# Performance work log

Hardware: AMD Instinct MI355X
Metric: run time of the kernel (lower is better)

The kernel has to match this reference:

```python
import math
import jax, jax.numpy as jnp
import numpy as np

G, PQ, PV = 12, 4, 8

def setup_inputs() -> dict:
    key = jax.random.key(0)
    ks = jax.random.split(key, 14)
    N, L, Cn, Ce, Ch = 1, 512, 384, 128, 192
    Node = jax.random.normal(ks[0], (N, L, Cn), jnp.float32)
    Edge = jax.random.normal(ks[1], (N, L, L, Ce), jnp.float32)
    # proper rotation matrices via QR of random gaussians
    raw = jax.random.normal(ks[2], (N, L, 3, 3), jnp.float32)
    rots, _ = jnp.linalg.qr(raw)
    trans = jax.random.normal(ks[3], (N, L, 3), jnp.float32) * 10.0
    def lin(k, fan_in, fan_out):
        return jax.random.normal(k, (fan_in, fan_out), jnp.float32) / np.sqrt(fan_in)
    return {
        'Node': Node, 'Edge': Edge, 'rots': rots, 'trans': trans,
        'Wq': lin(ks[4], Cn, Ch), 'Wk': lin(ks[5], Cn, Ch), 'Wv': lin(ks[6], Cn, Ch),
        'Wqv': lin(ks[7], Cn, 3 * G * PQ), 'Wkv': lin(ks[8], Cn, 3 * G * PQ),
        'Wvv': lin(ks[9], Cn, 3 * G * PV), 'Wbias': lin(ks[10], Ce, G),
        'gamma': jnp.zeros((G,), jnp.float32),
        'Wout': lin(ks[11], Ce * G + Ch + G * PV * 4, Cn),
        'bout': jnp.zeros((Cn,), jnp.float32),
    }

def reference(Node, Edge, rots, trans, Wq, Wk, Wv, Wqv, Wkv, Wvv, Wbias, gamma, Wout, bout):
    N, L, Cn = Node.shape
    Ce = Edge.shape[-1]
    Ch = Wq.shape[1]
    ppg = Ch // G
    t = trans / 10.0  # Frame(T.rots, T.trans / 10.0)
    q = (Node @ Wq).reshape(N, L, G, ppg)
    k = (Node @ Wk).reshape(N, L, G, ppg)
    v = (Node @ Wv).reshape(N, L, G, ppg)
    qv = (Node @ Wqv).reshape(N, L, G, PQ, 3)
    kv = (Node @ Wkv).reshape(N, L, G, PQ, 3)
    vv = (Node @ Wvv).reshape(N, L, G, PV, 3)
    apply_frame = lambda p: jnp.einsum('nlij,nlgpj->nlgpi', rots, p) + t[:, :, None, None]
    qv = apply_frame(qv)
    kv = apply_frame(kv)
    vv = apply_frame(vv)
    # pairwise squared point distances, summed over xyz and query points -> [N,L,L,G]
    d = qv[:, :, None] - kv[:, None]
    sq = jnp.sum(d * d, axis=(-1, -2))
    bias = jnp.einsum('nijc,cg->nijg', Edge, Wbias)
    WC = math.sqrt(2.0 / 9.0 / PQ)
    WL = math.sqrt(1.0 / 3.0)
    attn = jnp.einsum('nlgc,nmgc->nlmg', q, k) / math.sqrt(ppg) + bias
    attn = attn - jax.nn.softplus(gamma) * (WC / 2.0) * sq
    attn = jax.nn.softmax(WL * attn, axis=2)  # softmax over key index m
    O_Edge = jnp.einsum('nijg,nijc->nigc', attn, Edge).reshape(N, L, G * Ce)
    O_Node = jnp.einsum('nijg,njgc->nigc', attn, v).reshape(N, L, Ch)
    O_vec = jnp.einsum('nijg,njgpc->nigpc', attn, vv)
    # invert_apply: R^T (x - t)
    O_vec = jnp.einsum('nlji,nlgpj->nlgpi', rots, O_vec - t[:, :, None, None])
    O_norm = jnp.sqrt(jnp.sum(O_vec * O_vec, axis=-1) + 1e-8).reshape(N, L, -1)
    O_vec = O_vec.reshape(N, L, -1)
    feat = jnp.concatenate([O_Edge, O_Node, O_vec, O_norm], axis=-1)
    return feat @ Wout + bout
```

## Files before the change

kernel.cpp:

```cpp
#include <hip/hip_runtime.h>
#include <math.h>

#define LQ 512
#define CN 384
#define CE 128
#define CH 192
#define NG 12
#define PPG 16
#define FEAT 2112
#define NPROJ 1152

#define WS_RAW  0u
#define WS_QVG  589824u
#define WS_KVT  663552u
#define WS_VVG  737280u
#define WS_QN   884736u
#define WS_KNT  890880u
#define WS_KT   897024u
#define WS_ATT  995328u
#define WS_FEAT 4141056u
#define WS_PART 5222400u
#define WS_PM   WS_PART
#define WS_PS   (WS_PART + 12288u)

__global__ __launch_bounds__(256) void k1a_gemm(
    const float* __restrict__ Node,
    const float* __restrict__ Wq, const float* __restrict__ Wk,
    const float* __restrict__ Wv, const float* __restrict__ Wqv,
    const float* __restrict__ Wkv, const float* __restrict__ Wvv,
    float* __restrict__ ws)
{
    __shared__ float As[64][68];
    __shared__ float Bs[64][48];
    const int tid = threadIdx.x;
    const int cb = blockIdx.x % 24;
    const int l0 = (blockIdx.x / 24) * 64;
    const int col0 = cb * 48;

    const float* W; int nc, lc0;
    if (col0 < 192)      { W = Wq;  nc = 192; lc0 = col0; }
    else if (col0 < 384) { W = Wk;  nc = 192; lc0 = col0 - 192; }
    else if (col0 < 576) { W = Wv;  nc = 192; lc0 = col0 - 384; }
    else if (col0 < 720) { W = Wqv; nc = 144; lc0 = col0 - 576; }
    else if (col0 < 864) { W = Wkv; nc = 144; lc0 = col0 - 720; }
    else                 { W = Wvv; nc = 288; lc0 = col0 - 864; }

    const int tx = tid & 15, ty = tid >> 4;
    float acc[4][3];
#pragma unroll
    for (int r = 0; r < 4; ++r)
#pragma unroll
        for (int c = 0; c < 3; ++c) acc[r][c] = 0.f;

    for (int kc = 0; kc < 6; ++kc) {
        __syncthreads();
#pragma unroll
        for (int pass = 0; pass < 4; ++pass) {
            int m = (tid >> 4) + pass * 16;
            int kk = (tid & 15) * 4;
            const float4 a = *(const float4*)(Node + (size_t)(l0 + m) * CN + kc * 64 + kk);
            As[kk + 0][m] = a.x; As[kk + 1][m] = a.y;
            As[kk + 2][m] = a.z; As[kk + 3][m] = a.w;
        }
#pragma unroll
        for (int p = 0; p < 12; ++p) {
            int idx = p * 256 + tid;
            int kk = idx / 48, c = idx - kk * 48;
            Bs[kk][c] = W[(size_t)(kc * 64 + kk) * nc + lc0 + c];
        }
        __syncthreads();
#pragma unroll 8
        for (int kk = 0; kk < 64; ++kk) {
            const float4 av = *(const float4*)&As[kk][tx * 4];
            const float b0 = Bs[kk][ty * 3 + 0];
            const float b1 = Bs[kk][ty * 3 + 1];
            const float b2 = Bs[kk][ty * 3 + 2];
            acc[0][0] = fmaf(av.x, b0, acc[0][0]); acc[0][1] = fmaf(av.x, b1, acc[0][1]); acc[0][2] = fmaf(av.x, b2, acc[0][2]);
            acc[1][0] = fmaf(av.y, b0, acc[1][0]); acc[1][1] = fmaf(av.y, b1, acc[1][1]); acc[1][2] = fmaf(av.y, b2, acc[1][2]);
            acc[2][0] = fmaf(av.z, b0, acc[2][0]); acc[2][1] = fmaf(av.z, b1, acc[2][1]); acc[2][2] = fmaf(av.z, b2, acc[2][2]);
            acc[3][0] = fmaf(av.w, b0, acc[3][0]); acc[3][1] = fmaf(av.w, b1, acc[3][1]); acc[3][2] = fmaf(av.w, b2, acc[3][2]);
        }
    }
    float* raw = ws + WS_RAW;
#pragma unroll
    for (int r = 0; r < 4; ++r)
#pragma unroll
        for (int c = 0; c < 3; ++c)
            raw[(size_t)(l0 + tx * 4 + r) * NPROJ + col0 + ty * 3 + c] = acc[r][c];
    if (col0 >= 192 && col0 < 384) {
#pragma unroll
        for (int r = 0; r < 4; ++r)
#pragma unroll
            for (int c = 0; c < 3; ++c)
                ws[WS_KT + (size_t)(col0 - 192 + ty * 3 + c) * LQ + l0 + tx * 4 + r] = acc[r][c];
    }
}

__global__ __launch_bounds__(256) void k1b_vec(
    const float* __restrict__ rots, const float* __restrict__ trans,
    float* __restrict__ ws)
{
    __shared__ float sqbuf[96];
    const int tid = threadIdx.x;
    const int l = blockIdx.x;
    const float* raw = ws + WS_RAW + (size_t)l * NPROJ;

    if (tid < 192) {
        int src, pt, typ;
        if (tid < 48)      { typ = 0; pt = tid;      src = 576 + pt * 3; }
        else if (tid < 96) { typ = 1; pt = tid - 48; src = 720 + pt * 3; }
        else               { typ = 2; pt = tid - 96; src = 864 + pt * 3; }
        float v0 = raw[src], v1 = raw[src + 1], v2 = raw[src + 2];
        const float* R = rots + l * 9;
        float o0 = R[0] * v0 + R[1] * v1 + R[2] * v2 + trans[l * 3 + 0] * 0.1f;
        float o1 = R[3] * v0 + R[4] * v1 + R[5] * v2 + trans[l * 3 + 1] * 0.1f;
        float o2 = R[6] * v0 + R[7] * v1 + R[8] * v2 + trans[l * 3 + 2] * 0.1f;
        if (typ == 0) {
            float* dst = ws + WS_QVG + (size_t)l * 144 + pt * 3;
            dst[0] = o0; dst[1] = o1; dst[2] = o2;
        } else if (typ == 1) {
            ws[WS_KVT + (size_t)(pt * 3 + 0) * LQ + l] = o0;
            ws[WS_KVT + (size_t)(pt * 3 + 1) * LQ + l] = o1;
            ws[WS_KVT + (size_t)(pt * 3 + 2) * LQ + l] = o2;
        } else {
            float* dst = ws + WS_VVG + (size_t)l * 288 + pt * 3;
            dst[0] = o0; dst[1] = o1; dst[2] = o2;
        }
        if (tid < 96) sqbuf[tid] = o0 * o0 + o1 * o1 + o2 * o2;
    }
    __syncthreads();
    if (tid < 24) {
        int typ = tid / 12, g = tid % 12;
        int b = typ * 48 + g * 4;
        float s = sqbuf[b] + sqbuf[b + 1] + sqbuf[b + 2] + sqbuf[b + 3];
        if (typ == 0) ws[WS_QN + (size_t)l * 12 + g] = s;
        else          ws[WS_KNT + (size_t)g * LQ + l] = s;
    }
}

__global__ __launch_bounds__(256, 3) void k2_attn(
    const float* __restrict__ Edge, const float* __restrict__ Wbias,
    const float* __restrict__ gamma, float* __restrict__ ws)
{
    __shared__ float et[256 * 33];
    __shared__ float wbs[CE * NG];
    __shared__ float qls[CH], qvls[144], qnls[NG], cgls[NG];
    __shared__ float red[4][NG];
    const int tid = threadIdx.x;
    const int i = blockIdx.x >> 1;
    const int h = blockIdx.x & 1;
    const int j = h * 256 + tid;

    for (int u = tid; u < CE * NG; u += 256) wbs[u] = Wbias[u];
    if (tid < CH)  qls[tid]  = ws[WS_RAW + (size_t)i * NPROJ + tid];
    if (tid < 144) qvls[tid] = ws[WS_QVG + (size_t)i * 144 + tid];
    if (tid < NG) {
        qnls[tid] = ws[WS_QN + (size_t)i * NG + tid];
        cgls[tid] = log1pf(__expf(gamma[tid])) * 0.11785113019775793f;
    }
    __syncthreads();

    float lgs[NG];
    {
        const float* KT  = ws + WS_KT;
        const float* KVT = ws + WS_KVT;
        const float* KNT = ws + WS_KNT;
#pragma unroll
        for (int g = 0; g < NG; ++g) {
            float qk = 0.f;
#pragma unroll
            for (int u = 0; u < PPG; ++u)
                qk = fmaf(qls[g * PPG + u], KT[(size_t)(g * PPG + u) * LQ + j], qk);
            float dt = 0.f;
#pragma unroll
            for (int u = 0; u < 12; ++u)
                dt = fmaf(qvls[g * 12 + u], KVT[(size_t)(g * 12 + u) * LQ + j], dt);
            float sq = qnls[g] + KNT[(size_t)g * LQ + j] - 2.f * dt;
            lgs[g] = qk * 0.25f - cgls[g] * sq;
        }
    }

    const float4* e4 = (const float4*)Edge + ((size_t)i * LQ + h * 256) * 32;
    for (int ch = 0; ch < 4; ++ch) {
        __syncthreads();
#pragma unroll
        for (int kk = 0; kk < 8; ++kk) {
            int idx = kk * 256 + tid;
            int jr = idx >> 3, c4 = idx & 7;
            float4 v = e4[(size_t)jr * 32 + ch * 8 + c4];
            float* d = et + jr * 33 + c4 * 4;
            d[0] = v.x; d[1] = v.y; d[2] = v.z; d[3] = v.w;
        }
        __syncthreads();
        const float* wbch = wbs + ch * 32 * NG;
        const float* r0 = et + tid * 33;
#pragma unroll 4
        for (int c = 0; c < 32; ++c) {
            float e0 = r0[c];
            const float* wb = wbch + c * NG;
#pragma unroll
            for (int g = 0; g < NG; ++g) lgs[g] = fmaf(e0, wb[g], lgs[g]);
        }
    }

    const float WL = 0.5773502691896258f;
    const int wid = tid >> 6, lane = tid & 63;
    float pm[NG];
#pragma unroll
    for (int g = 0; g < NG; ++g) pm[g] = lgs[g];
#pragma unroll
    for (int g = 0; g < NG; ++g)
        for (int off = 1; off < 64; off <<= 1)
            pm[g] = fmaxf(pm[g], __shfl_xor(pm[g], off));
    if (lane == 0) {
#pragma unroll
        for (int g = 0; g < NG; ++g) red[wid][g] = pm[g];
    }
    __syncthreads();
    float gm[NG];
#pragma unroll
    for (int g = 0; g < NG; ++g)
        gm[g] = fmaxf(fmaxf(red[0][g], red[1][g]), fmaxf(red[2][g], red[3][g]));
    if (tid < NG)
        ws[WS_PM + ((size_t)i * 2 + h) * NG + tid] =
            fmaxf(fmaxf(red[0][tid], red[1][tid]), fmaxf(red[2][tid], red[3][tid]));
    __syncthreads();

    float ps[NG];
#pragma unroll
    for (int g = 0; g < NG; ++g) {
        float e = __expf(WL * (lgs[g] - gm[g]));
        lgs[g] = e;
        ps[g] = e;
    }
#pragma unroll
    for (int g = 0; g < NG; ++g)
        for (int off = 1; off < 64; off <<= 1)
            ps[g] += __shfl_xor(ps[g], off);
    if (lane == 0) {
#pragma unroll
        for (int g = 0; g < NG; ++g) red[wid][g] = ps[g];
    }
    __syncthreads();
    if (tid < NG)
        ws[WS_PS + ((size_t)i * 2 + h) * NG + tid] =
            red[0][tid] + red[1][tid] + red[2][tid] + red[3][tid];

    float4* dst = (float4*)(ws + WS_ATT + ((size_t)i * LQ + j) * NG);
    float4 s0, s1, s2;
    s0.x = lgs[0]; s0.y = lgs[1]; s0.z = lgs[2];  s0.w = lgs[3];
    s1.x = lgs[4]; s1.y = lgs[5]; s1.z = lgs[6];  s1.w = lgs[7];
    s2.x = lgs[8]; s2.y = lgs[9]; s2.z = lgs[10]; s2.w = lgs[11];
    dst[0] = s0; dst[1] = s1; dst[2] = s2;
}

__global__ __launch_bounds__(256) void k3_out(
    const float* __restrict__ Edge, const float* __restrict__ rots,
    const float* __restrict__ trans, float* __restrict__ ws)
{
    __shared__ float at[LQ][13];
    __shared__ float bufA[4][32][NG][4];
    __shared__ float ovec[288];
    __shared__ float sc[2][NG];
    const int tid = threadIdx.x;
    const int qi = blockIdx.x;
    const float* att = ws + WS_ATT + (size_t)qi * LQ * NG;

    if (tid < 24) {
        const float WL = 0.5773502691896258f;
        int hh = tid / NG, g = tid % NG;
        float m0 = ws[WS_PM + ((size_t)qi * 2 + 0) * NG + g];
        float m1 = ws[WS_PM + ((size_t)qi * 2 + 1) * NG + g];
        float ss0 = ws[WS_PS + ((size_t)qi * 2 + 0) * NG + g];
        float ss1 = ws[WS_PS + ((size_t)qi * 2 + 1) * NG + g];
        float m = fmaxf(m0, m1);
        float e0 = __expf(WL * (m0 - m));
        float e1 = __expf(WL * (m1 - m));
        float denom = ss0 * e0 + ss1 * e1;
        sc[hh][g] = (hh ? e1 : e0) / denom;
    }
    __syncthreads();

    for (int m = 0; m < 2; ++m) {
        int j = tid + m * 256;
        int hh = j >> 8;
        const float4* src = (const float4*)(att + (size_t)j * NG);
        float4 a = src[0], b = src[1], c = src[2];
        at[j][0] = a.x * sc[hh][0]; at[j][1] = a.y * sc[hh][1];
        at[j][2] = a.z * sc[hh][2]; at[j][3] = a.w * sc[hh][3];
        at[j][4] = b.x * sc[hh][4]; at[j][5] = b.y * sc[hh][5];
        at[j][6] = b.z * sc[hh][6]; at[j][7] = b.w * sc[hh][7];
        at[j][8] = c.x * sc[hh][8]; at[j][9] = c.y * sc[hh][9];
        at[j][10] = c.z * sc[hh][10]; at[j][11] = c.w * sc[hh][11];
    }
    __syncthreads();

    const int w = tid >> 6, lane = tid & 63, jh = lane >> 5, c4 = lane & 31;
    float acc[NG][4];
#pragma unroll
    for (int g = 0; g < NG; ++g)
#pragma unroll
        for (int r = 0; r < 4; ++r) acc[g][r] = 0.f;
    const float4* e4 = (const float4*)(Edge + (size_t)qi * LQ * CE);
    for (int jj = 0; jj < 64; ++jj) {
        int j = w * 128 + jh * 64 + jj;
        float4 e = e4[(size_t)j * 32 + c4];
#pragma unroll
        for (int g = 0; g < NG; ++g) {
            float a = at[j][g];
            acc[g][0] = fmaf(a, e.x, acc[g][0]);
            acc[g][1] = fmaf(a, e.y, acc[g][1]);
            acc[g][2] = fmaf(a, e.z, acc[g][2]);
            acc[g][3] = fmaf(a, e.w, acc[g][3]);
        }
    }
#pragma unroll
    for (int g = 0; g < NG; ++g)
#pragma unroll
        for (int r = 0; r < 4; ++r) acc[g][r] += __shfl_xor(acc[g][r], 32);
    if (jh == 0) {
#pragma unroll
        for (int g = 0; g < NG; ++g)
#pragma unroll
            for (int r = 0; r < 4; ++r) bufA[w][c4][g][r] = acc[g][r];
    }
    __syncthreads();
    float* feat = ws + WS_FEAT + (size_t)qi * FEAT;
    for (int m = 0; m < 6; ++m) {
        int o = tid + m * 256;
        int g = o >> 7, c = o & 127;
        int cc4 = c >> 2, r = c & 3;
        feat[o] = bufA[0][cc4][g][r] + bufA[1][cc4][g][r] +
                  bufA[2][cc4][g][r] + bufA[3][cc4][g][r];
    }

    const float* raw = ws + WS_RAW;
    const float* vvg = ws + WS_VVG;
    for (int ph = 0; ph < 2; ++ph) {
        int task = tid + ph * 256;
        if (task < 192) {
            int g = task >> 4;
            float s = 0.f;
            for (int j = 0; j < LQ; ++j) s = fmaf(at[j][g], raw[(size_t)j * NPROJ + 384 + task], s);
            feat[1536 + task] = s;
        } else if (task < 480) {
            int u = task - 192;
            int g = u / 24;
            float s = 0.f;
            for (int j = 0; j < LQ; ++j) s = fmaf(at[j][g], vvg[(size_t)j * 288 + u], s);
            ovec[u] = s;
        }
    }
    __syncthreads();

    if (tid < 96) {
        int g = tid >> 3, p = tid & 7;
        const float* R = rots + qi * 9;
        float t0 = trans[qi * 3 + 0] * 0.1f;
        float t1 = trans[qi * 3 + 1] * 0.1f;
        float t2 = trans[qi * 3 + 2] * 0.1f;
        float d0 = ovec[g * 24 + p * 3 + 0] - t0;
        float d1 = ovec[g * 24 + p * 3 + 1] - t1;
        float d2 = ovec[g * 24 + p * 3 + 2] - t2;
        float o0 = R[0] * d0 + R[3] * d1 + R[6] * d2;
        float o1 = R[1] * d0 + R[4] * d1 + R[7] * d2;
        float o2 = R[2] * d0 + R[5] * d1 + R[8] * d2;
        feat[1728 + g * 24 + p * 3 + 0] = o0;
        feat[1728 + g * 24 + p * 3 + 1] = o1;
        feat[1728 + g * 24 + p * 3 + 2] = o2;
        feat[2016 + g * 8 + p] = sqrtf(o0 * o0 + o1 * o1 + o2 * o2 + 1e-8f);
    }
}

__global__ __launch_bounds__(256) void k4_gemm(const float* __restrict__ Wout,
                                               float* __restrict__ ws)
{
    __shared__ float As[64][68];
    __shared__ float Bs[64][48];
    const int tid = threadIdx.x;
    const int cc = blockIdx.x >> 6;
    const int t  = blockIdx.x & 63;
    const int l0 = (t >> 3) * 64;
    const int col0 = (t & 7) * 48;
    const float* feat = ws + WS_FEAT;

    const int tx = tid & 15, ty = tid >> 4;
    float acc[4][3];
#pragma unroll
    for (int r = 0; r < 4; ++r)
#pragma unroll
        for (int c = 0; c < 3; ++c) acc[r][c] = 0.f;

    for (int kc = cc * 11; kc < cc * 11 + 11; ++kc) {
        __syncthreads();
#pragma unroll
        for (int pass = 0; pass < 4; ++pass) {
            int m = (tid >> 4) + pass * 16;
            int kk = (tid & 15) * 4;
            const float4 a = *(const float4*)(feat + (size_t)(l0 + m) * FEAT + kc * 64 + kk);
            As[kk + 0][m] = a.x; As[kk + 1][m] = a.y;
            As[kk + 2][m] = a.z; As[kk + 3][m] = a.w;
        }
#pragma unroll
        for (int p = 0; p < 12; ++p) {
            int idx = p * 256 + tid;
            int kk = idx / 48, c = idx - kk * 48;
            Bs[kk][c] = Wout[(size_t)(kc * 64 + kk) * CN + col0 + c];
        }
        __syncthreads();
#pragma unroll 8
        for (int kk = 0; kk < 64; ++kk) {
            const float4 av = *(const float4*)&As[kk][tx * 4];
            const float b0 = Bs[kk][ty * 3 + 0];
            const float b1 = Bs[kk][ty * 3 + 1];
            const float b2 = Bs[kk][ty * 3 + 2];
            acc[0][0] = fmaf(av.x, b0, acc[0][0]); acc[0][1] = fmaf(av.x, b1, acc[0][1]); acc[0][2] = fmaf(av.x, b2, acc[0][2]);
            acc[1][0] = fmaf(av.y, b0, acc[1][0]); acc[1][1] = fmaf(av.y, b1, acc[1][1]); acc[1][2] = fmaf(av.y, b2, acc[1][2]);
            acc[2][0] = fmaf(av.z, b0, acc[2][0]); acc[2][1] = fmaf(av.z, b1, acc[2][1]); acc[2][2] = fmaf(av.z, b2, acc[2][2]);
            acc[3][0] = fmaf(av.w, b0, acc[3][0]); acc[3][1] = fmaf(av.w, b1, acc[3][1]); acc[3][2] = fmaf(av.w, b2, acc[3][2]);
        }
    }
    float* part = ws + WS_PART + (size_t)cc * LQ * CN;
#pragma unroll
    for (int r = 0; r < 4; ++r)
#pragma unroll
        for (int c = 0; c < 3; ++c)
            part[(size_t)(l0 + tx * 4 + r) * CN + col0 + ty * 3 + c] = acc[r][c];
}

__global__ __launch_bounds__(384) void k5_red(const float* __restrict__ bout,
                                              const float* __restrict__ wsc,
                                              float* __restrict__ out)
{
    const int i = blockIdx.x, n = threadIdx.x;
    const float* part = wsc + WS_PART;
    size_t idx = (size_t)i * CN + n;
    size_t st = (size_t)LQ * CN;
    out[idx] = part[idx] + part[st + idx] + part[2 * st + idx] + bout[n];
}

extern "C" void kernel_launch(void* const* d_in, const int* in_sizes, int n_in,
                              void* d_out, int out_size, void* d_ws, size_t ws_size,
                              hipStream_t stream) {
    const float* Node  = (const float*)d_in[0];
    const float* Edge  = (const float*)d_in[1];
    const float* rots  = (const float*)d_in[2];
    const float* trans = (const float*)d_in[3];
    const float* Wq    = (const float*)d_in[4];
    const float* Wk    = (const float*)d_in[5];
    const float* Wv    = (const float*)d_in[6];
    const float* Wqv   = (const float*)d_in[7];
    const float* Wkv   = (const float*)d_in[8];
    const float* Wvv   = (const float*)d_in[9];
    const float* Wbias = (const float*)d_in[10];
    const float* gamma = (const float*)d_in[11];
    const float* Wout  = (const float*)d_in[12];
    const float* bout  = (const float*)d_in[13];
    float* ws = (float*)d_ws;

    k1a_gemm<<<192, 256, 0, stream>>>(Node, Wq, Wk, Wv, Wqv, Wkv, Wvv, ws);
    k1b_vec<<<512, 256, 0, stream>>>(rots, trans, ws);
    k2_attn<<<1024, 256, 0, stream>>>(Edge, Wbias, gamma, ws);
    k3_out<<<512, 256, 0, stream>>>(Edge, rots, trans, ws);
    k4_gemm<<<192, 256, 0, stream>>>(Wout, ws);
    k5_red<<<512, 384, 0, stream>>>(bout, ws, (float*)d_out);
}
```

Measured before the change: 207.2 us.

## Split attention logits kernel into quarter-row blocks and prefetch edge chunks into registers

```diff
diff --git a/kernel.cpp b/kernel.cpp
--- a/kernel.cpp
+++ b/kernel.cpp
@@ -21,7 +21,7 @@
 #define WS_FEAT 4141056u
 #define WS_PART 5222400u
 #define WS_PM   WS_PART
-#define WS_PS   (WS_PART + 12288u)
+#define WS_PS   (WS_PART + 24576u)
 
 __global__ __launch_bounds__(256) void k1a_gemm(
     const float* __restrict__ Node,
@@ -138,22 +138,22 @@
     }
 }
 
-__global__ __launch_bounds__(256, 3) void k2_attn(
+__global__ __launch_bounds__(128, 4) void k2_attn(
     const float* __restrict__ Edge, const float* __restrict__ Wbias,
     const float* __restrict__ gamma, float* __restrict__ ws)
 {
-    __shared__ float et[256 * 33];
+    __shared__ float et[128 * 33];
     __shared__ float wbs[CE * NG];
     __shared__ float qls[CH], qvls[144], qnls[NG], cgls[NG];
-    __shared__ float red[4][NG];
+    __shared__ float red[2][NG];
     const int tid = threadIdx.x;
-    const int i = blockIdx.x >> 1;
-    const int h = blockIdx.x & 1;
-    const int j = h * 256 + tid;
-
-    for (int u = tid; u < CE * NG; u += 256) wbs[u] = Wbias[u];
-    if (tid < CH)  qls[tid]  = ws[WS_RAW + (size_t)i * NPROJ + tid];
-    if (tid < 144) qvls[tid] = ws[WS_QVG + (size_t)i * 144 + tid];
+    const int i = blockIdx.x >> 2;
+    const int q = blockIdx.x & 3;
+    const int j = q * 128 + tid;
+
+    for (int u = tid; u < CE * NG; u += 128) wbs[u] = Wbias[u];
+    for (int u = tid; u < CH; u += 128)  qls[u]  = ws[WS_RAW + (size_t)i * NPROJ + u];
+    for (int u = tid; u < 144; u += 128) qvls[u] = ws[WS_QVG + (size_t)i * 144 + u];
     if (tid < NG) {
         qnls[tid] = ws[WS_QN + (size_t)i * NG + tid];
         cgls[tid] = log1pf(__expf(gamma[tid])) * 0.11785113019775793f;
@@ -180,18 +180,33 @@
         }
     }
 
-    const float4* e4 = (const float4*)Edge + ((size_t)i * LQ + h * 256) * 32;
+    const float4* ebase = (const float4*)Edge + ((size_t)i * LQ + q * 128) * 32;
+    float4 buf[8];
+#pragma unroll
+    for (int p = 0; p < 8; ++p) {
+        int idx = p * 128 + tid;
+        int jr = idx >> 3, c4 = idx & 7;
+        buf[p] = ebase[(size_t)jr * 32 + c4];
+    }
     for (int ch = 0; ch < 4; ++ch) {
         __syncthreads();
 #pragma unroll
-        for (int kk = 0; kk < 8; ++kk) {
-            int idx = kk * 256 + tid;
+        for (int p = 0; p < 8; ++p) {
+            int idx = p * 128 + tid;
             int jr = idx >> 3, c4 = idx & 7;
-            float4 v = e4[(size_t)jr * 32 + ch * 8 + c4];
+            float4 v = buf[p];
             float* d = et + jr * 33 + c4 * 4;
             d[0] = v.x; d[1] = v.y; d[2] = v.z; d[3] = v.w;
         }
         __syncthreads();
+        if (ch < 3) {
+#pragma unroll
+            for (int p = 0; p < 8; ++p) {
+                int idx = p * 128 + tid;
+                int jr = idx >> 3, c4 = idx & 7;
+                buf[p] = ebase[(size_t)jr * 32 + (ch + 1) * 8 + c4];
+            }
+        }
         const float* wbch = wbs + ch * 32 * NG;
         const float* r0 = et + tid * 33;
 #pragma unroll 4
@@ -219,11 +234,9 @@
     __syncthreads();
     float gm[NG];
 #pragma unroll
-    for (int g = 0; g < NG; ++g)
-        gm[g] = fmaxf(fmaxf(red[0][g], red[1][g]), fmaxf(red[2][g], red[3][g]));
+    for (int g = 0; g < NG; ++g) gm[g] = fmaxf(red[0][g], red[1][g]);
     if (tid < NG)
-        ws[WS_PM + ((size_t)i * 2 + h) * NG + tid] =
-            fmaxf(fmaxf(red[0][tid], red[1][tid]), fmaxf(red[2][tid], red[3][tid]));
+        ws[WS_PM + ((size_t)i * 4 + q) * NG + tid] = fmaxf(red[0][tid], red[1][tid]);
     __syncthreads();
 
     float ps[NG];
@@ -243,8 +256,7 @@
     }
     __syncthreads();
     if (tid < NG)
-        ws[WS_PS + ((size_t)i * 2 + h) * NG + tid] =
-            red[0][tid] + red[1][tid] + red[2][tid] + red[3][tid];
+        ws[WS_PS + ((size_t)i * 4 + q) * NG + tid] = red[0][tid] + red[1][tid];
 
     float4* dst = (float4*)(ws + WS_ATT + ((size_t)i * LQ + j) * NG);
     float4 s0, s1, s2;
@@ -261,29 +273,36 @@
     __shared__ float at[LQ][13];
     __shared__ float bufA[4][32][NG][4];
     __shared__ float ovec[288];
-    __shared__ float sc[2][NG];
+    __shared__ float sc[4][NG];
     const int tid = threadIdx.x;
     const int qi = blockIdx.x;
     const float* att = ws + WS_ATT + (size_t)qi * LQ * NG;
 
-    if (tid < 24) {
+    if (tid < 48) {
         const float WL = 0.5773502691896258f;
         int hh = tid / NG, g = tid % NG;
-        float m0 = ws[WS_PM + ((size_t)qi * 2 + 0) * NG + g];
-        float m1 = ws[WS_PM + ((size_t)qi * 2 + 1) * NG + g];
-        float ss0 = ws[WS_PS + ((size_t)qi * 2 + 0) * NG + g];
-        float ss1 = ws[WS_PS + ((size_t)qi * 2 + 1) * NG + g];
-        float m = fmaxf(m0, m1);
+        float m0 = ws[WS_PM + ((size_t)qi * 4 + 0) * NG + g];
+        float m1 = ws[WS_PM + ((size_t)qi * 4 + 1) * NG + g];
+        float m2 = ws[WS_PM + ((size_t)qi * 4 + 2) * NG + g];
+        float m3 = ws[WS_PM + ((size_t)qi * 4 + 3) * NG + g];
+        float s0 = ws[WS_PS + ((size_t)qi * 4 + 0) * NG + g];
+        float s1 = ws[WS_PS + ((size_t)qi * 4 + 1) * NG + g];
+        float s2 = ws[WS_PS + ((size_t)qi * 4 + 2) * NG + g];
+        float s3 = ws[WS_PS + ((size_t)qi * 4 + 3) * NG + g];
+        float m = fmaxf(fmaxf(m0, m1), fmaxf(m2, m3));
         float e0 = __expf(WL * (m0 - m));
         float e1 = __expf(WL * (m1 - m));
-        float denom = ss0 * e0 + ss1 * e1;
-        sc[hh][g] = (hh ? e1 : e0) / denom;
+        float e2 = __expf(WL * (m2 - m));
+        float e3 = __expf(WL * (m3 - m));
+        float denom = s0 * e0 + s1 * e1 + s2 * e2 + s3 * e3;
+        float eh = (hh == 0) ? e0 : (hh == 1) ? e1 : (hh == 2) ? e2 : e3;
+        sc[hh][g] = eh / denom;
     }
     __syncthreads();
 
     for (int m = 0; m < 2; ++m) {
         int j = tid + m * 256;
-        int hh = j >> 8;
+        int hh = j >> 7;
         const float4* src = (const float4*)(att + (size_t)j * NG);
         float4 a = src[0], b = src[1], c = src[2];
         at[j][0] = a.x * sc[hh][0]; at[j][1] = a.y * sc[hh][1];
@@ -460,7 +479,7 @@
 
     k1a_gemm<<<192, 256, 0, stream>>>(Node, Wq, Wk, Wv, Wqv, Wkv, Wvv, ws);
     k1b_vec<<<512, 256, 0, stream>>>(rots, trans, ws);
-    k2_attn<<<1024, 256, 0, stream>>>(Edge, Wbias, gamma, ws);
+    k2_attn<<<2048, 128, 0, stream>>>(Edge, Wbias, gamma, ws);
     k3_out<<<512, 256, 0, stream>>>(Edge, rots, trans, ws);
     k4_gemm<<<192, 256, 0, stream>>>(Wout, ws);
     k5_red<<<512, 384, 0, stream>>>(bout, ws, (float*)d_out);
```

Measured after the change: 220.9 us. 6.6% more time.
